# Optimization experiments

Measured on AMD Instinct MI355X. Metric: run time of the kernel, lower is better.

## Reference

```python
import jax, jax.numpy as jnp
import numpy as np

BS, S, D = 2, 2048, 1024
H = 16
DK = D // H  # 64
ROPE_BASE = 10000.0


def _rope(x):
    # x: [b, s, h, dk]; apply rotary embedding along s with per-pair angles.
    s, d = x.shape[1], x.shape[-1]
    theta = 1.0 / (ROPE_BASE ** (jnp.arange(0, d, 2, dtype=jnp.float32) / d))  # [d/2]
    ang = jnp.arange(s, dtype=jnp.float32)[:, None] * theta[None, :]            # [s, d/2]
    cos = jnp.cos(ang)[None, :, None, :]
    sin = jnp.sin(ang)[None, :, None, :]
    xs = x.reshape(*x.shape[:-1], d // 2, 2)
    x0, x1 = xs[..., 0], xs[..., 1]
    out = jnp.stack([x0 * cos - x1 * sin, x1 * cos + x0 * sin], axis=-1)
    return out.reshape(x.shape)


def setup_inputs() -> dict:
    key = jax.random.key(0)
    ks = jax.random.split(key, 7)
    w = 0.02
    return {
        "Q": jax.random.normal(ks[0], (BS, S, D), dtype=jnp.float32),
        "prev": jax.random.normal(ks[1], (BS, H, S, S), dtype=jnp.float32) * 0.1,
        "Wq": jax.random.normal(ks[2], (D, H * DK), dtype=jnp.float32) * w,
        "bq": jnp.zeros((H * DK,), dtype=jnp.float32),
        "Wk": jax.random.normal(ks[3], (D, H * DK), dtype=jnp.float32) * w,
        "bk": jnp.zeros((H * DK,), dtype=jnp.float32),
        "Wv": jax.random.normal(ks[4], (D, H * DK), dtype=jnp.float32) * w,
        "bv": jnp.zeros((H * DK,), dtype=jnp.float32),
        "Wo": jax.random.normal(ks[5], (H * DK, D), dtype=jnp.float32) * w,
        "bo": jnp.zeros((D,), dtype=jnp.float32),
    }


def reference(Q, prev, Wq, bq, Wk, bk, Wv, bv, Wo, bo):
    bs, s, _ = Q.shape
    scale = DK ** -0.5
    # QKV projections (self-attention: K = V = Q)
    q = (Q @ Wq + bq).reshape(bs, s, H, DK)
    k = (Q @ Wk + bk).reshape(bs, s, H, DK)
    v = (Q @ Wv + bv).reshape(bs, s, H, DK)
    # RoPE on q and k (per-call, matching the torch module)
    q = _rope(q)
    k = _rope(k)
    # scores with residual bias from previous layer
    attn_scores = jnp.einsum("bqhd,bkhd->bhqk", q, k) * scale + prev
    attn_weights = jax.nn.softmax(attn_scores, axis=-1)  # dropout p=0.0
    out = jnp.einsum("bhqk,bkhd->bqhd", attn_weights, v).reshape(bs, s, H * DK)
    out = out @ Wo + bo  # proj dropout p=0.0
    return out, attn_scores
```

## Files before the change

kernel.cpp:

```cpp
#include <hip/hip_runtime.h>
#include <hip/hip_bf16.h>
#include <math.h>
#include <cstdint>

#define S_LEN 2048
#define DKH 64

typedef __attribute__((ext_vector_type(8))) short s16x8;
typedef __attribute__((ext_vector_type(4))) float f32x4;

__device__ __forceinline__ unsigned short f2bf(float f) {
  unsigned int u = __float_as_uint(f);
  return (unsigned short)((u + 0x7fffu + ((u >> 16) & 1u)) >> 16);
}

__device__ __forceinline__ void glds16(const void* g, void* l) {
  __builtin_amdgcn_global_load_lds(
      (const __attribute__((address_space(1))) unsigned int*)(uintptr_t)g,
      (__attribute__((address_space(3))) unsigned int*)(uintptr_t)l, 16, 0, 0);
}

__global__ void k_rope_table(float* __restrict__ cosT, float* __restrict__ sinT) {
  int idx = blockIdx.x * 256 + threadIdx.x;
  if (idx >= S_LEN * 32) return;
  int s = idx >> 5, i = idx & 31;
  float theta = powf(10000.0f, -(float)i / 32.0f);
  float ang = (float)s * theta;
  float sv, cv;
  sincosf(ang, &sv, &cv);
  cosT[idx] = cv;
  sinT[idx] = sv;
}

__global__ __launch_bounds__(256) void k_wtrans4(const float* __restrict__ W0,
                                                 const float* __restrict__ W1,
                                                 const float* __restrict__ W2,
                                                 const float* __restrict__ W3,
                                                 unsigned short* __restrict__ WT) {
  __shared__ float t[32][33];
  const float* W = blockIdx.z == 0 ? W0 : (blockIdx.z == 1 ? W1 : (blockIdx.z == 2 ? W2 : W3));
  unsigned short* dst = WT + (size_t)blockIdx.z * 1048576;
  int n0 = blockIdx.x * 32, k0 = blockIdx.y * 32;
  int tx = threadIdx.x & 31, ty = threadIdx.x >> 5;
#pragma unroll
  for (int p = 0; p < 4; ++p)
    t[ty + p * 8][tx] = W[(size_t)(k0 + ty + p * 8) * 1024 + n0 + tx];
  __syncthreads();
#pragma unroll
  for (int p = 0; p < 4; ++p)
    dst[(size_t)(n0 + ty + p * 8) * 1024 + k0 + tx] = f2bf(t[tx][ty + p * 8]);
}

__global__ __launch_bounds__(256) void k_qconv(const float* __restrict__ Q,
                                               unsigned short* __restrict__ Qbf) {
  int idx = (blockIdx.x * 256 + threadIdx.x) * 8;
  float4 a = *(const float4*)(Q + idx);
  float4 b = *(const float4*)(Q + idx + 4);
  s16x8 o;
  o[0] = (short)f2bf(a.x); o[1] = (short)f2bf(a.y); o[2] = (short)f2bf(a.z); o[3] = (short)f2bf(a.w);
  o[4] = (short)f2bf(b.x); o[5] = (short)f2bf(b.y); o[6] = (short)f2bf(b.z); o[7] = (short)f2bf(b.w);
  *(s16x8*)(Qbf + idx) = o;
}

__global__ __launch_bounds__(256) void k_vtrans(const unsigned short* __restrict__ vl,
                                                unsigned short* __restrict__ vt) {
  __shared__ unsigned short t[64][65];
  int bh = blockIdx.y;
  int s0 = blockIdx.x * 64;
  int tx = threadIdx.x & 3;
  int r = threadIdx.x >> 2;
  const unsigned short* src = vl + (size_t)bh * S_LEN * DKH + (size_t)s0 * DKH;
  s16x8 a = *(const s16x8*)(src + r * 64 + tx * 16);
  s16x8 b = *(const s16x8*)(src + r * 64 + tx * 16 + 8);
#pragma unroll
  for (int j = 0; j < 8; ++j) { t[r][tx * 16 + j] = (unsigned short)a[j]; t[r][tx * 16 + 8 + j] = (unsigned short)b[j]; }
  __syncthreads();
  unsigned short* dst = vt + (size_t)bh * DKH * S_LEN + (size_t)r * S_LEN + s0;
  s16x8 o0, o1;
#pragma unroll
  for (int j = 0; j < 8; ++j) { o0[j] = (short)t[tx * 16 + j][r]; o1[j] = (short)t[tx * 16 + 8 + j][r]; }
  *(s16x8*)(dst + tx * 16) = o0;
  *(s16x8*)(dst + tx * 16 + 8) = o1;
}

__global__ __launch_bounds__(256) void k_qkv(
    const unsigned short* __restrict__ Qbf, const unsigned short* __restrict__ WTqkv,
    const float* __restrict__ bq, const float* __restrict__ bk, const float* __restrict__ bv,
    const float* __restrict__ cosT, const float* __restrict__ sinT,
    unsigned short* __restrict__ ql, unsigned short* __restrict__ kl,
    unsigned short* __restrict__ vl) {
  __shared__ unsigned short As[128 * 64];
  __shared__ unsigned short Bs[128 * 64];
  const int m0 = blockIdx.y * 128, n0 = blockIdx.x * 128;
  const int tid = threadIdx.x, lane = tid & 63, wave = tid >> 6;
  const int wm = (wave >> 1) * 64, wn = (wave & 1) * 64;
  const int lr = lane & 15, lg = lane >> 4;
  const int widx = n0 >> 10;
  const float* bias = widx == 0 ? bq : (widx == 1 ? bk : bv);
  const int lrow = lane >> 3, lcol = (lane & 7) * 8;

  f32x4 acc[4][4] = {};
  for (int k0 = 0; k0 < 1024; k0 += 64) {
    __syncthreads();
#pragma unroll
    for (int i = 0; i < 4; ++i) {
      int chunk = wave * 4 + i;
      glds16(Qbf + (size_t)(m0 + 8 * chunk + lrow) * 1024 + k0 + lcol, &As[chunk * 512]);
      glds16(WTqkv + (size_t)(n0 + 8 * chunk + lrow) * 1024 + k0 + lcol, &Bs[chunk * 512]);
    }
    __syncthreads();
#pragma unroll
    for (int ks = 0; ks < 2; ++ks) {
      s16x8 af[4], bf[4];
#pragma unroll
      for (int i = 0; i < 4; ++i) af[i] = *(const s16x8*)&As[(wm + i * 16 + lr) * 64 + ks * 32 + lg * 8];
#pragma unroll
      for (int i = 0; i < 4; ++i) bf[i] = *(const s16x8*)&Bs[(wn + i * 16 + lr) * 64 + ks * 32 + lg * 8];
#pragma unroll
      for (int mi = 0; mi < 4; ++mi)
#pragma unroll
        for (int ni = 0; ni < 4; ++ni)
          acc[mi][ni] = __builtin_amdgcn_mfma_f32_16x16x32_bf16(af[mi], bf[ni], acc[mi][ni], 0, 0, 0);
    }
  }

#pragma unroll
  for (int ni = 0; ni < 4; ++ni) {
    int n = n0 + wn + ni * 16 + lr;
    int np = n & 1023;
    float bval = bias[np];
    int h = np >> 6, d = np & 63;
    int ia = d >> 1;
#pragma unroll
    for (int mi = 0; mi < 4; ++mi) {
#pragma unroll
      for (int r = 0; r < 4; ++r) {
        int m = m0 + wm + mi * 16 + lg * 4 + r;
        int s = m & 2047, b = m >> 11;
        float val = acc[mi][ni][r] + bval;
        size_t oidx = ((size_t)(b * 16 + h) * 2048 + s) * 64 + d;
        if (widx == 2) {
          vl[oidx] = f2bf(val);
        } else {
          float part = __shfl_xor(val, 1);
          float c = cosT[s * 32 + ia], sn = sinT[s * 32 + ia];
          float outv = (d & 1) ? (val * c + part * sn) : (val * c - part * sn);
          (widx == 0 ? ql : kl)[oidx] = f2bf(outv);
        }
      }
    }
  }
}

__global__ __launch_bounds__(256, 4) void k_attn(
    const unsigned short* __restrict__ ql, const unsigned short* __restrict__ kl,
    const unsigned short* __restrict__ vt, const float* __restrict__ prev,
    float* __restrict__ scores, unsigned short* __restrict__ attn_out) {
  __shared__ unsigned short Ks[2][64 * 64];
  __shared__ unsigned short Vs[2][64 * 64];
  __shared__ unsigned short Ps[4][16 * 64];

  const int bid = blockIdx.x;
  const int xcd = bid & 7, idx = bid >> 3;
  const int bh = xcd * 4 + (idx >> 5);
  const int qb = idx & 31;

  const int tid = threadIdx.x, lane = tid & 63, wave = tid >> 6;
  const int lr = lane & 15, lg = lane >> 4;
  const int qw = qb * 64 + wave * 16;
  const int kr = lane >> 3, kc = lane & 7;

  s16x8 qf[2];
#pragma unroll
  for (int ks = 0; ks < 2; ++ks)
    qf[ks] = *(const s16x8*)(ql + ((size_t)bh * S_LEN + qw + lr) * DKH + ks * 32 + lg * 8);

  f32x4 o[4] = {};
  float m_run[4], l_run[4];
#pragma unroll
  for (int r = 0; r < 4; ++r) { m_run[r] = -1e30f; l_run[r] = 0.f; }

  const float scale = 0.125f;
  const unsigned short* kbase = kl + (size_t)bh * S_LEN * DKH;
  const unsigned short* vbase = vt + (size_t)bh * DKH * S_LEN;
  const float* prevB = prev + (size_t)bh * S_LEN * S_LEN;
  float* scoB = scores + (size_t)bh * S_LEN * S_LEN;
  unsigned short* PsW = &Ps[wave][0];

#pragma unroll
  for (int half = 0; half < 2; ++half) {
    const int rb = wave * 16 + half * 8;
    const int row = rb + kr;
    glds16(kbase + (size_t)row * DKH + ((kc ^ kr) * 8), &Ks[0][rb * 64]);
    glds16(vbase + (size_t)row * S_LEN + ((kc ^ kr) * 8), &Vs[0][rb * 64]);
  }
  asm volatile("s_waitcnt vmcnt(0)" ::: "memory");
  __builtin_amdgcn_s_barrier();

  for (int t = 0; t < 32; ++t) {
    const int cur = t & 1;
    const int kv0 = t * 64;
    const int kvn = ((t + 1) & 31) * 64;

    float pvv[16];
#pragma unroll
    for (int n = 0; n < 4; ++n)
#pragma unroll
      for (int r = 0; r < 4; ++r)
        pvv[n * 4 + r] = __builtin_nontemporal_load(
            prevB + (size_t)(qw + lg * 4 + r) * S_LEN + kv0 + n * 16 + lr);
    __builtin_amdgcn_sched_barrier(0);

#pragma unroll
    for (int half = 0; half < 2; ++half) {
      const int rb = wave * 16 + half * 8;
      const int row = rb + kr;
      glds16(kbase + (size_t)(kvn + row) * DKH + ((kc ^ kr) * 8), &Ks[cur ^ 1][rb * 64]);
      glds16(vbase + (size_t)row * S_LEN + kvn + ((kc ^ kr) * 8), &Vs[cur ^ 1][rb * 64]);
    }
    __builtin_amdgcn_sched_barrier(0);

    __builtin_amdgcn_s_setprio(1);
    f32x4 sc[4];
#pragma unroll
    for (int n = 0; n < 4; ++n) {
      f32x4 a = {};
#pragma unroll
      for (int ks = 0; ks < 2; ++ks) {
        s16x8 kf = *(const s16x8*)((const char*)&Ks[cur][0] + (n * 16 + lr) * 128 +
                                   ((ks * 64 + lg * 16) ^ ((lr & 7) << 4)));
        a = __builtin_amdgcn_mfma_f32_16x16x32_bf16(qf[ks], kf, a, 0, 0, 0);
      }
      sc[n] = a;
    }
    __builtin_amdgcn_s_setprio(0);

    float tmax[4] = {-1e30f, -1e30f, -1e30f, -1e30f};
#pragma unroll
    for (int n = 0; n < 4; ++n) {
      const int col = kv0 + n * 16 + lr;
#pragma unroll
      for (int r = 0; r < 4; ++r) {
        float v = sc[n][r] * scale + pvv[n * 4 + r];
        __builtin_nontemporal_store(v, scoB + (size_t)(qw + lg * 4 + r) * S_LEN + col);
        sc[n][r] = v;
        tmax[r] = fmaxf(tmax[r], v);
      }
    }
#pragma unroll
    for (int mask = 1; mask < 16; mask <<= 1)
#pragma unroll
      for (int r = 0; r < 4; ++r) tmax[r] = fmaxf(tmax[r], __shfl_xor(tmax[r], mask));

    bool small = true;
#pragma unroll
    for (int r = 0; r < 4; ++r) small = small && (tmax[r] <= m_run[r] + 8.0f);
    if (!__all(small)) {
#pragma unroll
      for (int r = 0; r < 4; ++r) {
        const float mn = fmaxf(m_run[r], tmax[r]);
        const float al = __expf(m_run[r] - mn);
        m_run[r] = mn;
        l_run[r] *= al;
#pragma unroll
        for (int df = 0; df < 4; ++df) o[df][r] *= al;
      }
    }

#pragma unroll
    for (int n = 0; n < 4; ++n)
#pragma unroll
      for (int r = 0; r < 4; ++r) {
        const float p = __expf(sc[n][r] - m_run[r]);
        l_run[r] += p;
        const int prow = lg * 4 + r;
        *(unsigned short*)((char*)PsW + prow * 128 +
                           ((n * 32 + lr * 2) ^ ((prow & 7) << 4))) = f2bf(p);
      }

    s16x8 pa[2];
#pragma unroll
    for (int ks = 0; ks < 2; ++ks)
      pa[ks] = *(const s16x8*)((const char*)PsW + lr * 128 +
                               ((ks * 64 + lg * 16) ^ ((lr & 7) << 4)));
    __builtin_amdgcn_s_setprio(1);
#pragma unroll
    for (int df = 0; df < 4; ++df) {
#pragma unroll
      for (int ks = 0; ks < 2; ++ks) {
        s16x8 vb = *(const s16x8*)((const char*)&Vs[cur][0] + (df * 16 + lr) * 128 +
                                   ((ks * 64 + lg * 16) ^ ((lr & 7) << 4)));
        o[df] = __builtin_amdgcn_mfma_f32_16x16x32_bf16(pa[ks], vb, o[df], 0, 0, 0);
      }
    }
    __builtin_amdgcn_s_setprio(0);

    asm volatile("s_waitcnt vmcnt(16)" ::: "memory");
    __builtin_amdgcn_s_barrier();
  }

#pragma unroll
  for (int mask = 1; mask < 16; mask <<= 1)
#pragma unroll
    for (int r = 0; r < 4; ++r) l_run[r] += __shfl_xor(l_run[r], mask);
  float inv[4];
#pragma unroll
  for (int r = 0; r < 4; ++r) inv[r] = 1.0f / l_run[r];

  const int b = bh >> 4, h = bh & 15;
#pragma unroll
  for (int df = 0; df < 4; ++df) {
    const int d = df * 16 + lr;
#pragma unroll
    for (int r = 0; r < 4; ++r) {
      const int row = qw + lg * 4 + r;
      attn_out[((size_t)(b * S_LEN + row)) * 1024 + h * 64 + d] = f2bf(o[df][r] * inv[r]);
    }
  }
}

__global__ __launch_bounds__(256) void k_outproj(
    const unsigned short* __restrict__ A, const unsigned short* __restrict__ WoT,
    const float* __restrict__ bo, float* __restrict__ out) {
  __shared__ unsigned short As[64 * 64];
  __shared__ unsigned short Bs[64 * 64];
  const int m0 = blockIdx.y * 64, n0 = blockIdx.x * 64;
  const int tid = threadIdx.x, lane = tid & 63, wave = tid >> 6;
  const int wm = (wave >> 1) * 32, wn = (wave & 1) * 32;
  const int lr = lane & 15, lg = lane >> 4;
  const int lrow = lane >> 3, lcol = (lane & 7) * 8;
  f32x4 acc[2][2] = {};
  for (int k0 = 0; k0 < 1024; k0 += 64) {
    __syncthreads();
#pragma unroll
    for (int i = 0; i < 2; ++i) {
      int chunk = wave * 2 + i;
      glds16(A + (size_t)(m0 + 8 * chunk + lrow) * 1024 + k0 + lcol, &As[chunk * 512]);
      glds16(WoT + (size_t)(n0 + 8 * chunk + lrow) * 1024 + k0 + lcol, &Bs[chunk * 512]);
    }
    __syncthreads();
#pragma unroll
    for (int ks = 0; ks < 2; ++ks) {
      s16x8 af[2], bf[2];
#pragma unroll
      for (int i = 0; i < 2; ++i) af[i] = *(const s16x8*)&As[(wm + i * 16 + lr) * 64 + ks * 32 + lg * 8];
#pragma unroll
      for (int i = 0; i < 2; ++i) bf[i] = *(const s16x8*)&Bs[(wn + i * 16 + lr) * 64 + ks * 32 + lg * 8];
#pragma unroll
      for (int mi = 0; mi < 2; ++mi)
#pragma unroll
        for (int ni = 0; ni < 2; ++ni)
          acc[mi][ni] = __builtin_amdgcn_mfma_f32_16x16x32_bf16(af[mi], bf[ni], acc[mi][ni], 0, 0, 0);
    }
  }
#pragma unroll
  for (int ni = 0; ni < 2; ++ni) {
    int n = n0 + wn + ni * 16 + lr;
    float bv = bo[n];
#pragma unroll
    for (int mi = 0; mi < 2; ++mi)
#pragma unroll
      for (int rr = 0; rr < 4; ++rr) {
        int m = m0 + wm + mi * 16 + lg * 4 + rr;
        out[(size_t)m * 1024 + n] = acc[mi][ni][rr] + bv;
      }
  }
}

extern "C" void kernel_launch(void* const* d_in, const int* in_sizes, int n_in,
                              void* d_out, int out_size, void* d_ws, size_t ws_size,
                              hipStream_t stream) {
  const float* Q = (const float*)d_in[0];
  const float* prev = (const float*)d_in[1];
  const float* Wq = (const float*)d_in[2];
  const float* bq = (const float*)d_in[3];
  const float* Wk = (const float*)d_in[4];
  const float* bk = (const float*)d_in[5];
  const float* Wv = (const float*)d_in[6];
  const float* bv = (const float*)d_in[7];
  const float* Wo = (const float*)d_in[8];
  const float* bo = (const float*)d_in[9];

  float* out = (float*)d_out;
  float* scores = out + (size_t)4194304;

  char* ws = (char*)d_ws;
  float* cosT = (float*)ws;
  float* sinT = cosT + 65536;
  unsigned short* WTqkv = (unsigned short*)(ws + 524288);
  unsigned short* WoT = WTqkv + 3145728;
  unsigned short* ql = WoT + 1048576;
  unsigned short* kl = ql + 4194304;
  unsigned short* vl = kl + 4194304;
  unsigned short* vt = vl + 4194304;
  unsigned short* attn_out = vt + 4194304;
  unsigned short* Qbf = attn_out + 4194304;

  k_rope_table<<<256, 256, 0, stream>>>(cosT, sinT);
  k_wtrans4<<<dim3(32, 32, 4), 256, 0, stream>>>(Wq, Wk, Wv, Wo, WTqkv);
  k_qconv<<<2048, 256, 0, stream>>>(Q, Qbf);
  k_qkv<<<dim3(24, 32), 256, 0, stream>>>(Qbf, WTqkv, bq, bk, bv, cosT, sinT, ql, kl, vl);
  k_vtrans<<<dim3(32, 32), 256, 0, stream>>>(vl, vt);
  k_attn<<<1024, 256, 0, stream>>>(ql, kl, vt, prev, scores, attn_out);
  k_outproj<<<dim3(16, 64), 256, 0, stream>>>(attn_out, WoT, bo, out);
}
```

Measured before the change: 365.9 us.

## Stage prev bias through async LDS double buffer and load K/V directly to registers

The attention kernel stops staging K and V tiles in shared memory. Each wave now loads its K and V fragments straight from global memory into registers. The freed LDS is reused as a double-buffered area that async global-to-LDS copies fill with the per-wave prev bias tile for the next iteration, and the per-iteration block barrier and explicit vmcnt wait are removed. The aim is to prefetch the dominant prev stream earlier and drop block synchronisation. The cost is that K/V are fetched four times per block (once per wave) through cache, and correct ordering of the async prev copies now relies on implicit vmcnt waits.

After: 602.7 us. +64.7%, slower.

```diff
diff --git a/kernel.cpp b/kernel.cpp
--- a/kernel.cpp
+++ b/kernel.cpp
@@ -156,8 +156,7 @@
     const unsigned short* __restrict__ ql, const unsigned short* __restrict__ kl,
     const unsigned short* __restrict__ vt, const float* __restrict__ prev,
     float* __restrict__ scores, unsigned short* __restrict__ attn_out) {
-  __shared__ unsigned short Ks[2][64 * 64];
-  __shared__ unsigned short Vs[2][64 * 64];
+  __shared__ float Pv[2][64 * 64];
   __shared__ unsigned short Ps[4][16 * 64];
 
   const int bid = blockIdx.x;
@@ -168,7 +167,7 @@
   const int tid = threadIdx.x, lane = tid & 63, wave = tid >> 6;
   const int lr = lane & 15, lg = lane >> 4;
   const int qw = qb * 64 + wave * 16;
-  const int kr = lane >> 3, kc = lane & 7;
+  const int pr = lane >> 4, pc = lane & 15;
 
   s16x8 qf[2];
 #pragma unroll
@@ -188,35 +187,29 @@
   unsigned short* PsW = &Ps[wave][0];
 
 #pragma unroll
-  for (int half = 0; half < 2; ++half) {
-    const int rb = wave * 16 + half * 8;
-    const int row = rb + kr;
-    glds16(kbase + (size_t)row * DKH + ((kc ^ kr) * 8), &Ks[0][rb * 64]);
-    glds16(vbase + (size_t)row * S_LEN + ((kc ^ kr) * 8), &Vs[0][rb * 64]);
-  }
-  asm volatile("s_waitcnt vmcnt(0)" ::: "memory");
-  __builtin_amdgcn_s_barrier();
+  for (int i = 0; i < 4; ++i) {
+    const int row = qw + i * 4 + pr;
+    glds16(prevB + (size_t)row * S_LEN + pc * 4, &Pv[0][(wave * 16 + i * 4) * 64]);
+  }
 
   for (int t = 0; t < 32; ++t) {
     const int cur = t & 1;
     const int kv0 = t * 64;
     const int kvn = ((t + 1) & 31) * 64;
 
-    float pvv[16];
+    s16x8 kf[8];
 #pragma unroll
     for (int n = 0; n < 4; ++n)
 #pragma unroll
-      for (int r = 0; r < 4; ++r)
-        pvv[n * 4 + r] = __builtin_nontemporal_load(
-            prevB + (size_t)(qw + lg * 4 + r) * S_LEN + kv0 + n * 16 + lr);
+      for (int ks = 0; ks < 2; ++ks)
+        kf[n * 2 + ks] =
+            *(const s16x8*)(kbase + (size_t)(kv0 + n * 16 + lr) * DKH + ks * 32 + lg * 8);
     __builtin_amdgcn_sched_barrier(0);
 
 #pragma unroll
-    for (int half = 0; half < 2; ++half) {
-      const int rb = wave * 16 + half * 8;
-      const int row = rb + kr;
-      glds16(kbase + (size_t)(kvn + row) * DKH + ((kc ^ kr) * 8), &Ks[cur ^ 1][rb * 64]);
-      glds16(vbase + (size_t)row * S_LEN + kvn + ((kc ^ kr) * 8), &Vs[cur ^ 1][rb * 64]);
+    for (int i = 0; i < 4; ++i) {
+      const int row = qw + i * 4 + pr;
+      glds16(prevB + (size_t)row * S_LEN + kvn + pc * 4, &Pv[cur ^ 1][(wave * 16 + i * 4) * 64]);
     }
     __builtin_amdgcn_sched_barrier(0);
 
@@ -226,22 +219,29 @@
     for (int n = 0; n < 4; ++n) {
       f32x4 a = {};
 #pragma unroll
-      for (int ks = 0; ks < 2; ++ks) {
-        s16x8 kf = *(const s16x8*)((const char*)&Ks[cur][0] + (n * 16 + lr) * 128 +
-                                   ((ks * 64 + lg * 16) ^ ((lr & 7) << 4)));
-        a = __builtin_amdgcn_mfma_f32_16x16x32_bf16(qf[ks], kf, a, 0, 0, 0);
-      }
+      for (int ks = 0; ks < 2; ++ks)
+        a = __builtin_amdgcn_mfma_f32_16x16x32_bf16(qf[ks], kf[n * 2 + ks], a, 0, 0, 0);
       sc[n] = a;
     }
     __builtin_amdgcn_s_setprio(0);
 
+    s16x8 vf[8];
+#pragma unroll
+    for (int df = 0; df < 4; ++df)
+#pragma unroll
+      for (int ks = 0; ks < 2; ++ks)
+        vf[df * 2 + ks] =
+            *(const s16x8*)(vbase + (size_t)(df * 16 + lr) * S_LEN + kv0 + ks * 32 + lg * 8);
+    __builtin_amdgcn_sched_barrier(0);
+
+    const float* PvC = &Pv[cur][wave * 16 * 64];
     float tmax[4] = {-1e30f, -1e30f, -1e30f, -1e30f};
 #pragma unroll
     for (int n = 0; n < 4; ++n) {
       const int col = kv0 + n * 16 + lr;
 #pragma unroll
       for (int r = 0; r < 4; ++r) {
-        float v = sc[n][r] * scale + pvv[n * 4 + r];
+        float v = sc[n][r] * scale + PvC[(lg * 4 + r) * 64 + n * 16 + lr];
         __builtin_nontemporal_store(v, scoB + (size_t)(qw + lg * 4 + r) * S_LEN + col);
         sc[n][r] = v;
         tmax[r] = fmaxf(tmax[r], v);
@@ -285,18 +285,11 @@
                                ((ks * 64 + lg * 16) ^ ((lr & 7) << 4)));
     __builtin_amdgcn_s_setprio(1);
 #pragma unroll
-    for (int df = 0; df < 4; ++df) {
-#pragma unroll
-      for (int ks = 0; ks < 2; ++ks) {
-        s16x8 vb = *(const s16x8*)((const char*)&Vs[cur][0] + (df * 16 + lr) * 128 +
-                                   ((ks * 64 + lg * 16) ^ ((lr & 7) << 4)));
-        o[df] = __builtin_amdgcn_mfma_f32_16x16x32_bf16(pa[ks], vb, o[df], 0, 0, 0);
-      }
-    }
+    for (int df = 0; df < 4; ++df)
+#pragma unroll
+      for (int ks = 0; ks < 2; ++ks)
+        o[df] = __builtin_amdgcn_mfma_f32_16x16x32_bf16(pa[ks], vf[df * 2 + ks], o[df], 0, 0, 0);
     __builtin_amdgcn_s_setprio(0);
-
-    asm volatile("s_waitcnt vmcnt(16)" ::: "memory");
-    __builtin_amdgcn_s_barrier();
   }
 
 #pragma unroll
```
